# Kernel optimization log

Hardware: AMD Instinct MI355X
Metric: run time of the kernel (lower is better)

Reference implementation:

```python
import jax, jax.numpy as jnp
import numpy as np

N = 33_554_432
NUM_CLASSES = 10


def setup_inputs() -> dict:
    key = jax.random.key(0)
    k1, k2, k3 = jax.random.split(key, 3)
    predictions = jax.random.normal(k1, (N,), dtype=jnp.float32)
    labels = jax.random.randint(k2, (N,), 0, NUM_CLASSES, dtype=jnp.int32)
    weights = jax.random.uniform(k3, (NUM_CLASSES,), dtype=jnp.float32)
    return {"predictions": predictions, "labels": labels, "weights": weights}


def reference(predictions, labels, weights):
    # per-element weighted squared error: weights[label] * (pred - label)^2, then mean
    diff = predictions - labels.astype(predictions.dtype)
    w = weights[labels]  # gather per-class weight
    return jnp.mean(w * diff * diff)
```

## Files before the change

### kernel.cpp

```cpp
#include <hip/hip_runtime.h>

#define NBLOCKS 2048
#define NTHREADS 256

__global__ __launch_bounds__(NTHREADS) void wmse_partial_kernel(
    const float4* __restrict__ pred4,
    const int4* __restrict__ lab4,
    const float* __restrict__ weights,
    double* __restrict__ partials,
    int n4)
{
    __shared__ float w[16];
    if (threadIdx.x < 10) w[threadIdx.x] = weights[threadIdx.x];
    __syncthreads();

    double acc = 0.0;
    int idx = blockIdx.x * NTHREADS + threadIdx.x;
    const int stride = NBLOCKS * NTHREADS;

    for (int i = idx; i < n4; i += stride) {
        float4 p = pred4[i];
        int4 l = lab4[i];
        float d0 = p.x - (float)l.x;
        float d1 = p.y - (float)l.y;
        float d2 = p.z - (float)l.z;
        float d3 = p.w - (float)l.w;
        float s = w[l.x] * d0 * d0
                + w[l.y] * d1 * d1
                + w[l.z] * d2 * d2
                + w[l.w] * d3 * d3;
        acc += (double)s;
    }

    for (int off = 32; off > 0; off >>= 1)
        acc += __shfl_down(acc, off, 64);

    __shared__ double wave_sums[NTHREADS / 64];
    int lane = threadIdx.x & 63;
    int wid  = threadIdx.x >> 6;
    if (lane == 0) wave_sums[wid] = acc;
    __syncthreads();

    if (threadIdx.x == 0) {
        double t = 0.0;
        #pragma unroll
        for (int k = 0; k < NTHREADS / 64; ++k) t += wave_sums[k];
        partials[blockIdx.x] = t;
    }
}

__global__ __launch_bounds__(NTHREADS) void wmse_final_kernel(
    const double* __restrict__ partials,
    float* __restrict__ out,
    int nparts,
    double inv_n)
{
    double acc = 0.0;
    for (int i = threadIdx.x; i < nparts; i += NTHREADS)
        acc += partials[i];

    for (int off = 32; off > 0; off >>= 1)
        acc += __shfl_down(acc, off, 64);

    __shared__ double wave_sums[NTHREADS / 64];
    int lane = threadIdx.x & 63;
    int wid  = threadIdx.x >> 6;
    if (lane == 0) wave_sums[wid] = acc;
    __syncthreads();

    if (threadIdx.x == 0) {
        double t = 0.0;
        #pragma unroll
        for (int k = 0; k < NTHREADS / 64; ++k) t += wave_sums[k];
        out[0] = (float)(t * inv_n);
    }
}

extern "C" void kernel_launch(void* const* d_in, const int* in_sizes, int n_in,
                              void* d_out, int out_size, void* d_ws, size_t ws_size,
                              hipStream_t stream) {
    const float* pred    = (const float*)d_in[0];
    const int*   labels  = (const int*)d_in[1];
    const float* weights = (const float*)d_in[2];
    float* out = (float*)d_out;

    int n  = in_sizes[0];
    int n4 = n >> 2;

    double* partials = (double*)d_ws;

    wmse_partial_kernel<<<NBLOCKS, NTHREADS, 0, stream>>>(
        (const float4*)pred, (const int4*)labels, weights, partials, n4);

    wmse_final_kernel<<<1, NTHREADS, 0, stream>>>(
        partials, out, NBLOCKS, 1.0 / (double)n);
}
```

Baseline: 280.5 us.

## Fuse final reduction via atomicAdd and batch loads in a specialized fast path

Drops the second single-block reduction kernel and has each block atomically add its scaled partial sum into the output, which is zeroed with a memset first. A specialized path for the exact size (16 float4 per thread) issues 4 independent float4/int4 loads per batch, increasing memory-level parallelism, and accumulates in float within each batch of 4 loads. The change trades a kernel launch for a memset plus 2048 float atomics. It also introduces non-deterministic float summation order and reduced precision at the atomic stage.

```diff
diff --git a/kernel.cpp b/kernel.cpp
--- a/kernel.cpp
+++ b/kernel.cpp
@@ -2,34 +2,64 @@
 
 #define NBLOCKS 2048
 #define NTHREADS 256
+#define PER_THREAD 16
+#define BATCH 4
 
-__global__ __launch_bounds__(NTHREADS) void wmse_partial_kernel(
+__global__ __launch_bounds__(NTHREADS) void wmse_kernel(
     const float4* __restrict__ pred4,
     const int4* __restrict__ lab4,
     const float* __restrict__ weights,
-    double* __restrict__ partials,
-    int n4)
+    float* __restrict__ out,
+    int n4, double inv_n)
 {
     __shared__ float w[16];
     if (threadIdx.x < 10) w[threadIdx.x] = weights[threadIdx.x];
     __syncthreads();
 
+    const int stride = NBLOCKS * NTHREADS;
+    const int base = blockIdx.x * NTHREADS + threadIdx.x;
+
     double acc = 0.0;
-    int idx = blockIdx.x * NTHREADS + threadIdx.x;
-    const int stride = NBLOCKS * NTHREADS;
 
-    for (int i = idx; i < n4; i += stride) {
-        float4 p = pred4[i];
-        int4 l = lab4[i];
-        float d0 = p.x - (float)l.x;
-        float d1 = p.y - (float)l.y;
-        float d2 = p.z - (float)l.z;
-        float d3 = p.w - (float)l.w;
-        float s = w[l.x] * d0 * d0
-                + w[l.y] * d1 * d1
-                + w[l.z] * d2 * d2
-                + w[l.w] * d3 * d3;
-        acc += (double)s;
+    if (n4 == stride * PER_THREAD) {
+        #pragma unroll 1
+        for (int b = 0; b < PER_THREAD / BATCH; ++b) {
+            float4 p[BATCH];
+            int4   l[BATCH];
+            #pragma unroll
+            for (int k = 0; k < BATCH; ++k) {
+                int i = base + (b * BATCH + k) * stride;
+                p[k] = pred4[i];
+                l[k] = lab4[i];
+            }
+            float s = 0.f;
+            #pragma unroll
+            for (int k = 0; k < BATCH; ++k) {
+                float d0 = p[k].x - (float)l[k].x;
+                float d1 = p[k].y - (float)l[k].y;
+                float d2 = p[k].z - (float)l[k].z;
+                float d3 = p[k].w - (float)l[k].w;
+                s += w[l[k].x] * d0 * d0;
+                s += w[l[k].y] * d1 * d1;
+                s += w[l[k].z] * d2 * d2;
+                s += w[l[k].w] * d3 * d3;
+            }
+            acc += (double)s;
+        }
+    } else {
+        for (int i = base; i < n4; i += stride) {
+            float4 p = pred4[i];
+            int4 l = lab4[i];
+            float d0 = p.x - (float)l.x;
+            float d1 = p.y - (float)l.y;
+            float d2 = p.z - (float)l.z;
+            float d3 = p.w - (float)l.w;
+            float s = w[l.x] * d0 * d0
+                    + w[l.y] * d1 * d1
+                    + w[l.z] * d2 * d2
+                    + w[l.w] * d3 * d3;
+            acc += (double)s;
+        }
     }
 
     for (int off = 32; off > 0; off >>= 1)
@@ -45,34 +75,7 @@
         double t = 0.0;
         #pragma unroll
         for (int k = 0; k < NTHREADS / 64; ++k) t += wave_sums[k];
-        partials[blockIdx.x] = t;
-    }
-}
-
-__global__ __launch_bounds__(NTHREADS) void wmse_final_kernel(
-    const double* __restrict__ partials,
-    float* __restrict__ out,
-    int nparts,
-    double inv_n)
-{
-    double acc = 0.0;
-    for (int i = threadIdx.x; i < nparts; i += NTHREADS)
-        acc += partials[i];
-
-    for (int off = 32; off > 0; off >>= 1)
-        acc += __shfl_down(acc, off, 64);
-
-    __shared__ double wave_sums[NTHREADS / 64];
-    int lane = threadIdx.x & 63;
-    int wid  = threadIdx.x >> 6;
-    if (lane == 0) wave_sums[wid] = acc;
-    __syncthreads();
-
-    if (threadIdx.x == 0) {
-        double t = 0.0;
-        #pragma unroll
-        for (int k = 0; k < NTHREADS / 64; ++k) t += wave_sums[k];
-        out[0] = (float)(t * inv_n);
+        atomicAdd(out, (float)(t * inv_n));
     }
 }
 
@@ -87,11 +90,9 @@
     int n  = in_sizes[0];
     int n4 = n >> 2;
 
-    double* partials = (double*)d_ws;
+    hipMemsetAsync(out, 0, out_size * sizeof(float), stream);
 
-    wmse_partial_kernel<<<NBLOCKS, NTHREADS, 0, stream>>>(
-        (const float4*)pred, (const int4*)labels, weights, partials, n4);
-
-    wmse_final_kernel<<<1, NTHREADS, 0, stream>>>(
-        partials, out, NBLOCKS, 1.0 / (double)n);
+    wmse_kernel<<<NBLOCKS, NTHREADS, 0, stream>>>(
+        (const float4*)pred, (const int4*)labels, weights, out,
+        n4, 1.0 / (double)n);
 }
```

Result: no change. 282.1 us (+0.5%).

## Use 8192 blocks with fully unrolled nontemporal loads for exact-size fast path

Applied to the files above, without the earlier changes.

Raises the grid to 8192 blocks. When the element count exactly matches four strides, each thread issues all eight 16-byte loads up front using nontemporal loads, then computes with no loop. This aims to put more memory requests in flight and to keep the streamed data from polluting the cache. The fast path only fires for one exact size and falls back to the generic loop otherwise. It also quadruples the number of partials the final kernel must reduce.

```diff
diff --git a/kernel.cpp b/kernel.cpp
--- a/kernel.cpp
+++ b/kernel.cpp
@@ -1,11 +1,21 @@
 #include <hip/hip_runtime.h>
 
-#define NBLOCKS 2048
+#define NBLOCKS 8192
 #define NTHREADS 256
 
-__global__ __launch_bounds__(NTHREADS) void wmse_partial_kernel(
-    const float4* __restrict__ pred4,
-    const int4* __restrict__ lab4,
+typedef float fvec4 __attribute__((ext_vector_type(4)));
+typedef int   ivec4 __attribute__((ext_vector_type(4)));
+
+__device__ __forceinline__ fvec4 ntloadf(const fvec4* p) {
+    return __builtin_nontemporal_load(p);
+}
+__device__ __forceinline__ ivec4 ntloadi(const ivec4* p) {
+    return __builtin_nontemporal_load(p);
+}
+
+__global__ __launch_bounds__(NTHREADS) void wmse_kernel(
+    const fvec4* __restrict__ pred4,
+    const ivec4* __restrict__ lab4,
     const float* __restrict__ weights,
     double* __restrict__ partials,
     int n4)
@@ -14,22 +24,52 @@
     if (threadIdx.x < 10) w[threadIdx.x] = weights[threadIdx.x];
     __syncthreads();
 
+    const int stride = NBLOCKS * NTHREADS;
+    const int t = blockIdx.x * NTHREADS + threadIdx.x;
+
     double acc = 0.0;
-    int idx = blockIdx.x * NTHREADS + threadIdx.x;
-    const int stride = NBLOCKS * NTHREADS;
 
-    for (int i = idx; i < n4; i += stride) {
-        float4 p = pred4[i];
-        int4 l = lab4[i];
-        float d0 = p.x - (float)l.x;
-        float d1 = p.y - (float)l.y;
-        float d2 = p.z - (float)l.z;
-        float d3 = p.w - (float)l.w;
-        float s = w[l.x] * d0 * d0
-                + w[l.y] * d1 * d1
-                + w[l.z] * d2 * d2
-                + w[l.w] * d3 * d3;
-        acc += (double)s;
+    if (n4 == stride * 4) {
+        fvec4 p0 = ntloadf(pred4 + t);
+        fvec4 p1 = ntloadf(pred4 + t + stride);
+        fvec4 p2 = ntloadf(pred4 + t + 2 * stride);
+        fvec4 p3 = ntloadf(pred4 + t + 3 * stride);
+        ivec4 l0 = ntloadi(lab4 + t);
+        ivec4 l1 = ntloadi(lab4 + t + stride);
+        ivec4 l2 = ntloadi(lab4 + t + 2 * stride);
+        ivec4 l3 = ntloadi(lab4 + t + 3 * stride);
+
+        float s0, s1, s2, s3;
+        {
+            float d0 = p0.x - (float)l0.x, d1 = p0.y - (float)l0.y;
+            float d2 = p0.z - (float)l0.z, d3 = p0.w - (float)l0.w;
+            s0 = w[l0.x]*d0*d0 + w[l0.y]*d1*d1 + w[l0.z]*d2*d2 + w[l0.w]*d3*d3;
+        }
+        {
+            float d0 = p1.x - (float)l1.x, d1 = p1.y - (float)l1.y;
+            float d2 = p1.z - (float)l1.z, d3 = p1.w - (float)l1.w;
+            s1 = w[l1.x]*d0*d0 + w[l1.y]*d1*d1 + w[l1.z]*d2*d2 + w[l1.w]*d3*d3;
+        }
+        {
+            float d0 = p2.x - (float)l2.x, d1 = p2.y - (float)l2.y;
+            float d2 = p2.z - (float)l2.z, d3 = p2.w - (float)l2.w;
+            s2 = w[l2.x]*d0*d0 + w[l2.y]*d1*d1 + w[l2.z]*d2*d2 + w[l2.w]*d3*d3;
+        }
+        {
+            float d0 = p3.x - (float)l3.x, d1 = p3.y - (float)l3.y;
+            float d2 = p3.z - (float)l3.z, d3 = p3.w - (float)l3.w;
+            s3 = w[l3.x]*d0*d0 + w[l3.y]*d1*d1 + w[l3.z]*d2*d2 + w[l3.w]*d3*d3;
+        }
+        acc = (double)((s0 + s1) + (s2 + s3));
+    } else {
+        for (int i = t; i < n4; i += stride) {
+            fvec4 p = pred4[i];
+            ivec4 l = lab4[i];
+            float d0 = p.x - (float)l.x, d1 = p.y - (float)l.y;
+            float d2 = p.z - (float)l.z, d3 = p.w - (float)l.w;
+            acc += (double)(w[l.x]*d0*d0 + w[l.y]*d1*d1
+                          + w[l.z]*d2*d2 + w[l.w]*d3*d3);
+        }
     }
 
     for (int off = 32; off > 0; off >>= 1)
@@ -42,10 +82,10 @@
     __syncthreads();
 
     if (threadIdx.x == 0) {
-        double t = 0.0;
+        double tsum = 0.0;
         #pragma unroll
-        for (int k = 0; k < NTHREADS / 64; ++k) t += wave_sums[k];
-        partials[blockIdx.x] = t;
+        for (int k = 0; k < NTHREADS / 64; ++k) tsum += wave_sums[k];
+        partials[blockIdx.x] = tsum;
     }
 }
 
@@ -89,8 +129,8 @@
 
     double* partials = (double*)d_ws;
 
-    wmse_partial_kernel<<<NBLOCKS, NTHREADS, 0, stream>>>(
-        (const float4*)pred, (const int4*)labels, weights, partials, n4);
+    wmse_kernel<<<NBLOCKS, NTHREADS, 0, stream>>>(
+        (const fvec4*)pred, (const ivec4*)labels, weights, partials, n4);
 
     wmse_final_kernel<<<1, NTHREADS, 0, stream>>>(
         partials, out, NBLOCKS, 1.0 / (double)n);
```

After: 261.3 us. -6.9%, faster.
